# Kernel tuning notes

Measured on AMD Instinct MI355X. Metric: run time of the kernel, lower is better.

Reference implementation:

```python
import jax, jax.numpy as jnp
import numpy as np

L, B, T, C, H, FF = 2, 2, 2048, 512, 8, 1024
HS = C // H  # head size
EPS = 1.1920929e-07  # torch float32 finfo eps (nn.RMSNorm default)


def setup_inputs() -> dict:
    key = jax.random.key(0)
    ks = jax.random.split(key, 20)
    s = 0.02
    return {
        "hidden": jax.random.normal(ks[0], (B, T, C), jnp.float32),
        "target": jax.random.normal(ks[1], (B, T, C), jnp.float32),
        # self-attn per-head projections (bias=False)
        "Wq_s": jax.random.normal(ks[2], (L, H, C, HS)) * s,
        "Wk_s": jax.random.normal(ks[3], (L, H, C, HS)) * s,
        "Wv_s": jax.random.normal(ks[4], (L, H, C, HS)) * s,
        "Wo_s": jax.random.normal(ks[5], (L, C, C)) * s,
        "bo_s": jnp.zeros((L, C)),
        # cross-attn per-head projections
        "Wq_x": jax.random.normal(ks[6], (L, H, C, HS)) * s,
        "Wk_x": jax.random.normal(ks[7], (L, H, C, HS)) * s,
        "Wv_x": jax.random.normal(ks[8], (L, H, C, HS)) * s,
        "Wo_x": jax.random.normal(ks[9], (L, C, C)) * s,
        "bo_x": jnp.zeros((L, C)),
        # FFN
        "W1": jax.random.normal(ks[10], (L, C, FF)) * s,
        "b1": jnp.zeros((L, FF)),
        "W2": jax.random.normal(ks[11], (L, FF, C)) * s,
        "b2": jnp.zeros((L, C)),
        # RMSNorm gains ln1..ln4
        "g1": jnp.ones((L, C)),
        "g2": jnp.ones((L, C)),
        "g3": jnp.ones((L, C)),
        "g4": jnp.ones((L, C)),
    }


def _rms(x, g):
    return x * jax.lax.rsqrt(jnp.mean(x * x, axis=-1, keepdims=True) + EPS) * g


def _attn(q_in, kv_in, Wq, Wk, Wv, Wo, bo, causal):
    # q_in: [B,Tq,C], kv_in: [B,Tk,C]; W*: [H,C,HS]
    q = jnp.einsum('btc,hcd->bhtd', q_in, Wq)
    k = jnp.einsum('bsc,hcd->bhsd', kv_in, Wk)
    v = jnp.einsum('bsc,hcd->bhsd', kv_in, Wv)
    wei = jnp.einsum('bhtd,bhsd->bhts', q, k) * (HS ** -0.5)  # [B,H,Tq,Tk]
    if causal:
        Tq, Tk = q_in.shape[1], kv_in.shape[1]
        mask = jnp.tril(jnp.ones((Tq, Tk), bool))
        wei = jnp.where(mask, wei, -jnp.inf)
    wei = jax.nn.softmax(wei, axis=-1)
    out = jnp.einsum('bhts,bhsd->bhtd', wei, v)
    out = out.transpose(0, 2, 1, 3).reshape(q_in.shape[0], q_in.shape[1], C)
    return out @ Wo + bo


def reference(hidden, target, Wq_s, Wk_s, Wv_s, Wo_s, bo_s,
              Wq_x, Wk_x, Wv_x, Wo_x, bo_x,
              W1, b1, W2, b2, g1, g2, g3, g4):
    t = target
    for l in range(L):
        # masked self-attention with RMSNorm pre-norm + residual
        t = t + _attn(_rms(t, g1[l]), _rms(t, g1[l]), Wq_s[l], Wk_s[l], Wv_s[l],
                      Wo_s[l], bo_s[l], causal=True)
        # cross-attention: K/V from ln2(hidden), Q from ln3(t)
        t = t + _attn(_rms(t, g3[l]), _rms(hidden, g2[l]), Wq_x[l], Wk_x[l], Wv_x[l],
                      Wo_x[l], bo_x[l], causal=False)
        # GELU FFN
        h = _rms(t, g4[l])
        t = t + (jax.nn.gelu(h @ W1[l] + b1[l], approximate=False) @ W2[l] + b2[l])
    return t
```

## Files before the change

kernel.cpp:

```cpp
#include <hip/hip_runtime.h>
#include <hip/hip_bf16.h>
#include <math.h>

#define L 2
#define B 2
#define T 2048
#define C 512
#define H 8
#define FF 1024
#define HS 64
#define EPSV 1.1920929e-07f

typedef __hip_bfloat16 bf16;
typedef __attribute__((ext_vector_type(8))) short short8;
typedef __attribute__((ext_vector_type(4))) float f32x4;

__device__ __forceinline__ float b2f(bf16 x) { return __bfloat162float(x); }

__device__ __forceinline__ void gl16(const unsigned short* g, unsigned short* l) {
    __builtin_amdgcn_global_load_lds(
        (const __attribute__((address_space(1))) unsigned int*)g,
        (__attribute__((address_space(3))) unsigned int*)l, 16, 0, 0);
}

__global__ void detect_k(const unsigned short* __restrict__ g1bits, int* __restrict__ flag) {
    if (threadIdx.x == 0 && blockIdx.x == 0)
        *flag = (g1bits[0] != (unsigned short)0x3F80u) ? 1 : 0;
}

__device__ __forceinline__ float ld_in(const void* p, size_t i, int fl) {
    return fl ? ((const float*)p)[i] : b2f(((const bf16*)p)[i]);
}

#define QKVT_TOT 1572864
#define WO_TOT 524288
#define W12_TOT 1048576
#define SM_TOT 9216
#define ACT_TOT 2097152
#define PREP_TOT (2 * QKVT_TOT + 2 * WO_TOT + 2 * W12_TOT + SM_TOT + 2 * ACT_TOT)

struct PrepArgs {
    const void *Wq_s, *Wk_s, *Wv_s, *Wo_s, *Wq_x, *Wk_x, *Wv_x, *Wo_x, *W1, *W2;
    const void* sm[8];
    const void *hidden, *target;
    bf16 *cQKVs, *cQKVx, *cWoTs, *cWoTx, *cW1T, *cW2T, *smallDst;
    float *hid, *t_buf;
    const int* flag;
};

__global__ void prep_k(PrepArgs pa) {
    long long i = (long long)blockIdx.x * 256 + threadIdx.x;
    if (i >= PREP_TOT) return;
    int fl = *pa.flag;
    if (i < 2LL * QKVT_TOT) {
        int which = i >= QKVT_TOT;
        int j = (int)(i - (long long)which * QKVT_TOT);
        int l = j / 786432, r = j - l * 786432;
        int n = r >> 9, c = r & 511;
        int p = n >> 9, nn = n & 511;
        int hh = nn >> 6, d = nn & 63;
        const void* src = which ? (p == 0 ? pa.Wq_x : p == 1 ? pa.Wk_x : pa.Wv_x)
                                : (p == 0 ? pa.Wq_s : p == 1 ? pa.Wk_s : pa.Wv_s);
        size_t si = ((size_t)(l * 8 + hh) * 512 + c) * 64 + d;
        (which ? pa.cQKVx : pa.cQKVs)[j] = __float2bfloat16(ld_in(src, si, fl));
        return;
    }
    i -= 2LL * QKVT_TOT;
    if (i < 2LL * WO_TOT) {
        int which = i >= WO_TOT;
        int j = (int)(i - (long long)which * WO_TOT);
        int l = j >> 18, r = j & 262143;
        int n = r >> 9, c = r & 511;
        size_t si = ((size_t)l << 18) + ((size_t)c << 9) + n;
        (which ? pa.cWoTx : pa.cWoTs)[j] = __float2bfloat16(ld_in(which ? pa.Wo_x : pa.Wo_s, si, fl));
        return;
    }
    i -= 2LL * WO_TOT;
    if (i < W12_TOT) {
        int j = (int)i;
        int l = j >> 19, r = j & 524287;
        int n = r >> 9, c = r & 511;
        size_t si = ((size_t)l << 19) + ((size_t)c << 10) + n;
        pa.cW1T[j] = __float2bfloat16(ld_in(pa.W1, si, fl));
        return;
    }
    i -= W12_TOT;
    if (i < W12_TOT) {
        int j = (int)i;
        int l = j >> 19, r = j & 524287;
        int n = r >> 10, c = r & 1023;
        size_t si = ((size_t)l << 19) + ((size_t)c << 9) + n;
        pa.cW2T[j] = __float2bfloat16(ld_in(pa.W2, si, fl));
        return;
    }
    i -= W12_TOT;
    if (i < SM_TOT) {
        int j = (int)i;
        const int cum[9] = {0, 1024, 2048, 4096, 5120, 6144, 7168, 8192, 9216};
        int k = 0;
        while (j >= cum[k + 1]) k++;
        pa.smallDst[j] = __float2bfloat16(ld_in(pa.sm[k], j - cum[k], fl));
        return;
    }
    i -= SM_TOT;
    if (i < ACT_TOT) {
        pa.hid[i] = ld_in(pa.hidden, (size_t)i, fl);
    } else {
        size_t j = i - ACT_TOT;
        pa.t_buf[j] = ld_in(pa.target, j, fl);
    }
}

__global__ void write_out_k(const float* __restrict__ in, void* __restrict__ out, int n,
                            const int* __restrict__ flag) {
    int i = blockIdx.x * blockDim.x + threadIdx.x;
    if (i >= n) return;
    if (*flag) ((float*)out)[i] = in[i];
    else       ((bf16*)out)[i] = __float2bfloat16(in[i]);
}

__global__ void rmsnorm_k(const float* __restrict__ x, const bf16* __restrict__ g,
                          bf16* __restrict__ y) {
    int row = blockIdx.x;
    int tid = threadIdx.x;
    const float* xr = x + (size_t)row * C;
    float v0 = xr[tid], v1 = xr[tid + 256];
    __shared__ float red[256];
    red[tid] = v0 * v0 + v1 * v1;
    __syncthreads();
    for (int s = 128; s > 0; s >>= 1) {
        if (tid < s) red[tid] += red[tid + s];
        __syncthreads();
    }
    float sc = rsqrtf(red[0] / (float)C + EPSV);
    y[(size_t)row * C + tid] = __float2bfloat16(v0 * sc * b2f(g[tid]));
    y[(size_t)row * C + tid + 256] = __float2bfloat16(v1 * sc * b2f(g[tid + 256]));
}

__global__ void rmsnorm2_k(const float* __restrict__ xa, const bf16* __restrict__ ga,
                           bf16* __restrict__ ya, const float* __restrict__ xb,
                           const bf16* __restrict__ gb, bf16* __restrict__ yb) {
    int sel = blockIdx.y;
    const float* x = sel ? xb : xa;
    const bf16* g = sel ? gb : ga;
    bf16* y = sel ? yb : ya;
    int row = blockIdx.x;
    int tid = threadIdx.x;
    const float* xr = x + (size_t)row * C;
    float v0 = xr[tid], v1 = xr[tid + 256];
    __shared__ float red[256];
    red[tid] = v0 * v0 + v1 * v1;
    __syncthreads();
    for (int s = 128; s > 0; s >>= 1) {
        if (tid < s) red[tid] += red[tid + s];
        __syncthreads();
    }
    float sc = rsqrtf(red[0] / (float)C + EPSV);
    y[(size_t)row * C + tid] = __float2bfloat16(v0 * sc * b2f(g[tid]));
    y[(size_t)row * C + tid + 256] = __float2bfloat16(v1 * sc * b2f(g[tid + 256]));
}

#define GPAD 40
struct GDesc {
    const bf16* A; const bf16* Bt; const bf16* bias; float* resid; bf16* out;
    int N, K, ldOut, ep, nblkx, blkofs;
};
struct GBatch { GDesc d[3]; int nd; };

__global__ __launch_bounds__(256) void gemm_batch_k(GBatch gb) {
    int bid = blockIdx.x;
    int di = 0;
    if (gb.nd > 1 && bid >= gb.d[1].blkofs) di = 1;
    if (gb.nd > 2 && bid >= gb.d[2].blkofs) di = 2;
    GDesc g = gb.d[di];
    int lb = bid - g.blkofs;
    int bx = lb % g.nblkx, by = lb / g.nblkx;
    int m0 = by * 64, n0 = bx * 64;

    __shared__ unsigned short As[2][64 * GPAD], Bs[2][64 * GPAD];
    int tid = threadIdx.x, lane = tid & 63, wave = tid >> 6;
    int wr = wave >> 1, wc = wave & 1, quad = lane >> 4, l15 = lane & 15;
    const unsigned short* Au = (const unsigned short*)g.A;
    const unsigned short* Bu = (const unsigned short*)g.Bt;

    int srow = tid >> 2;
    int sseg = tid & 3;
    const unsigned short* agp = Au + (size_t)(m0 + srow) * g.K + sseg * 8;
    const unsigned short* bgp = Bu + (size_t)(n0 + srow) * g.K + sseg * 8;
    int soff = srow * GPAD + sseg * 8;

    short8 va = *(const short8*)agp;
    short8 vb = *(const short8*)bgp;
    *(short8*)(&As[0][soff]) = va;
    *(short8*)(&Bs[0][soff]) = vb;

    f32x4 zf = {0.f, 0.f, 0.f, 0.f};
    f32x4 acc[2][2];
    acc[0][0] = zf; acc[0][1] = zf; acc[1][0] = zf; acc[1][1] = zf;

    int ra0 = wr * 32 + l15, ra1 = ra0 + 16;
    int rb0 = wc * 32 + l15, rb1 = rb0 + 16;
    int oa0 = ra0 * GPAD + quad * 8;
    int oa1 = ra1 * GPAD + quad * 8;
    int ob0 = rb0 * GPAD + quad * 8;
    int ob1 = rb1 * GPAD + quad * 8;

    int nk = g.K >> 5;
    __syncthreads();
    for (int kt = 0; kt < nk; kt++) {
        int cur = kt & 1;
        if (kt + 1 < nk) {
            va = *(const short8*)(agp + (kt + 1) * 32);
            vb = *(const short8*)(bgp + (kt + 1) * 32);
        }
        short8 a0 = *(const short8*)(&As[cur][oa0]);
        short8 a1 = *(const short8*)(&As[cur][oa1]);
        short8 b0 = *(const short8*)(&Bs[cur][ob0]);
        short8 b1 = *(const short8*)(&Bs[cur][ob1]);
        acc[0][0] = __builtin_amdgcn_mfma_f32_16x16x32_bf16(a0, b0, acc[0][0], 0, 0, 0);
        acc[0][1] = __builtin_amdgcn_mfma_f32_16x16x32_bf16(a0, b1, acc[0][1], 0, 0, 0);
        acc[1][0] = __builtin_amdgcn_mfma_f32_16x16x32_bf16(a1, b0, acc[1][0], 0, 0, 0);
        acc[1][1] = __builtin_amdgcn_mfma_f32_16x16x32_bf16(a1, b1, acc[1][1], 0, 0, 0);
        if (kt + 1 < nk) {
            *(short8*)(&As[cur ^ 1][soff]) = va;
            *(short8*)(&Bs[cur ^ 1][soff]) = vb;
        }
        __syncthreads();
    }

#pragma unroll
    for (int mi = 0; mi < 2; mi++) {
#pragma unroll
        for (int ni = 0; ni < 2; ni++) {
            int colg = n0 + wc * 32 + ni * 16 + l15;
            float bv = (g.ep == 1 || g.ep == 2) ? b2f(g.bias[colg]) : 0.f;
#pragma unroll
            for (int r2 = 0; r2 < 4; r2++) {
                int rowg = m0 + wr * 32 + mi * 16 + quad * 4 + r2;
                float v = acc[mi][ni][r2];
                if (g.ep == 0) {
                    g.out[(size_t)rowg * g.ldOut + colg] = __float2bfloat16(v);
                } else if (g.ep == 1) {
                    g.resid[(size_t)rowg * g.ldOut + colg] += v + bv;
                } else if (g.ep == 2) {
                    float u = v + bv;
                    g.out[(size_t)rowg * g.ldOut + colg] =
                        __float2bfloat16(0.5f * u * (1.f + erff(u * 0.70710678118654752f)));
                } else {
                    g.out[((size_t)((colg >> 11) * 512 + rowg) << 11) + (colg & 2047)] =
                        __float2bfloat16(v);
                }
            }
        }
    }
}

#define PST 72
__global__ __launch_bounds__(256) void attn_mfma_k(const bf16* __restrict__ qkv,
                                                   const bf16* __restrict__ vT,
                                                   bf16* __restrict__ attnout, int causal) {
    __shared__ unsigned short KsA[2][4096], VtA[2][4096];
    __shared__ unsigned short Ps[4][16 * PST];
    int qt = causal ? (gridDim.x - 1 - blockIdx.x) : blockIdx.x;
    int h = blockIdx.y, b = blockIdx.z;
    int tid = threadIdx.x, lane = tid & 63, w = tid >> 6;
    int quad = lane >> 4, l15 = lane & 15;
    const unsigned short* qk = (const unsigned short*)qkv;
    const unsigned short* vTp = (const unsigned short*)vT + ((size_t)b * 512 + h * 64) * T;
    size_t rowbase = (size_t)b * T;
    int koff = 512 + h * 64;
    unsigned short* Pw = Ps[w];
    bf16* Pwb = (bf16*)Pw;

    const unsigned short* qrow = qk + (rowbase + qt * 64 + w * 16 + l15) * 1536 + h * 64;
    short8 aq0 = *(const short8*)(qrow + quad * 8);
    short8 aq1 = *(const short8*)(qrow + 32 + quad * 8);

    int srow = lane >> 3;
    int ssp = (lane & 7) ^ (srow & 7);

    f32x4 zf = {0.f, 0.f, 0.f, 0.f};
    f32x4 oacc[4];
#pragma unroll
    for (int i = 0; i < 4; i++) oacc[i] = zf;
    float lpart[4] = {0.f, 0.f, 0.f, 0.f};

    int nT = causal ? (qt + 1) : (T / 64);

#pragma unroll
    for (int j = 0; j < 2; j++) {
        int c = w * 2 + j;
        int r = c * 8 + srow;
        gl16(qk + (rowbase + r) * 1536 + koff + ssp * 8, KsA[0] + c * 512);
        gl16(vTp + (size_t)r * T + ssp * 8, VtA[0] + c * 512);
    }
    __syncthreads();

    int buf = 0;
    for (int st = 0; st < nT; st++) {
        if (st + 1 < nT) {
#pragma unroll
            for (int j = 0; j < 2; j++) {
                int c = w * 2 + j;
                int r = c * 8 + srow;
                gl16(qk + (rowbase + (st + 1) * 64 + r) * 1536 + koff + ssp * 8,
                     KsA[buf ^ 1] + c * 512);
                gl16(vTp + (size_t)r * T + (st + 1) * 64 + ssp * 8, VtA[buf ^ 1] + c * 512);
            }
        }

        const unsigned short* Kb = KsA[buf];
        const unsigned short* Vb = VtA[buf];

        f32x4 sacc[4];
#pragma unroll
        for (int i = 0; i < 4; i++) sacc[i] = zf;
#pragma unroll
        for (int ni = 0; ni < 4; ni++) {
            int rr = ni * 16 + l15;
            short8 bk0 = *(const short8*)(Kb + rr * 64 + ((quad ^ (rr & 7)) * 8));
            short8 bk1 = *(const short8*)(Kb + rr * 64 + (((4 + quad) ^ (rr & 7)) * 8));
            sacc[ni] = __builtin_amdgcn_mfma_f32_16x16x32_bf16(aq0, bk0, sacc[ni], 0, 0, 0);
            sacc[ni] = __builtin_amdgcn_mfma_f32_16x16x32_bf16(aq1, bk1, sacc[ni], 0, 0, 0);
        }

        bool diag = causal && (st == qt);
        int qrl = w * 16 + quad * 4;
#pragma unroll
        for (int reg = 0; reg < 4; reg++) {
            float lp = 0.f;
#pragma unroll
            for (int ni = 0; ni < 4; ni++) {
                int s_l = ni * 16 + l15;
                float p = __expf(sacc[ni][reg] * 0.125f);
                if (diag && s_l > qrl + reg) p = 0.f;
                lp += p;
                Pwb[(quad * 4 + reg) * PST + s_l] = __float2bfloat16(p);
            }
            lpart[reg] += lp;
        }

        short8 ap0 = *(const short8*)(Pw + l15 * PST + quad * 8);
        short8 ap1 = *(const short8*)(Pw + l15 * PST + 32 + quad * 8);
#pragma unroll
        for (int dj = 0; dj < 4; dj++) {
            int rr = dj * 16 + l15;
            short8 bv0 = *(const short8*)(Vb + rr * 64 + ((quad ^ (rr & 7)) * 8));
            short8 bv1 = *(const short8*)(Vb + rr * 64 + (((4 + quad) ^ (rr & 7)) * 8));
            oacc[dj] = __builtin_amdgcn_mfma_f32_16x16x32_bf16(ap0, bv0, oacc[dj], 0, 0, 0);
            oacc[dj] = __builtin_amdgcn_mfma_f32_16x16x32_bf16(ap1, bv1, oacc[dj], 0, 0, 0);
        }

        __syncthreads();
        buf ^= 1;
    }

#pragma unroll
    for (int reg = 0; reg < 4; reg++) {
#pragma unroll
        for (int mk = 1; mk < 16; mk <<= 1) lpart[reg] += __shfl_xor(lpart[reg], mk, 64);
        lpart[reg] = 1.0f / lpart[reg];
    }
#pragma unroll
    for (int dj = 0; dj < 4; dj++) {
        int d = dj * 16 + l15;
#pragma unroll
        for (int reg = 0; reg < 4; reg++) {
            int q = w * 16 + quad * 4 + reg;
            attnout[(rowbase + qt * 64 + q) * C + h * HS + d] =
                __float2bfloat16(oacc[dj][reg] * lpart[reg]);
        }
    }
}

extern "C" void kernel_launch(void* const* d_in, const int* in_sizes, int n_in,
                              void* d_out, int out_size, void* d_ws, size_t ws_size,
                              hipStream_t stream) {
    const int BTC = B * T * C;
    const int BTF = B * T * FF;

    char* wsb = (char*)d_ws;
    int* flag = (int*)wsb;
    bf16* cur = (bf16*)(wsb + 256);
    bf16* cQKVs = cur;   cur += QKVT_TOT;
    bf16* cQKVx = cur;   cur += QKVT_TOT;
    bf16* cWoTs = cur;   cur += WO_TOT;
    bf16* cWoTx = cur;   cur += WO_TOT;
    bf16* cW1T = cur;    cur += W12_TOT;
    bf16* cW2T = cur;    cur += W12_TOT;
    bf16* smallBase = cur;
    bf16* cbo_s = cur;   cur += L * C;
    bf16* cbo_x = cur;   cur += L * C;
    bf16* cb1 = cur;     cur += L * FF;
    bf16* cb2 = cur;     cur += L * C;
    bf16* cg1 = cur;     cur += L * C;
    bf16* cg2 = cur;     cur += L * C;
    bf16* cg3 = cur;     cur += L * C;
    bf16* cg4 = cur;     cur += L * C;
    bf16* n1 = cur;      cur += BTC;
    bf16* n2 = cur;      cur += BTC;
    bf16* qkvbuf = cur;  cur += B * T * 3 * C;
    bf16* vTbuf = cur;   cur += BTC;
    bf16* attnout = cur; cur += BTC;
    bf16* h1buf = cur;   cur += BTF;
    size_t f32_off = (((char*)cur - wsb) + 255) & ~(size_t)255;
    float* t_buf = (float*)(wsb + f32_off);
    float* hid = t_buf + BTC;

    dim3 blk256(256);
    detect_k<<<1, 64, 0, stream>>>((const unsigned short*)d_in[16], flag);

    PrepArgs pa;
    pa.Wq_s = d_in[2]; pa.Wk_s = d_in[3]; pa.Wv_s = d_in[4]; pa.Wo_s = d_in[5];
    pa.Wq_x = d_in[7]; pa.Wk_x = d_in[8]; pa.Wv_x = d_in[9]; pa.Wo_x = d_in[10];
    pa.W1 = d_in[12]; pa.W2 = d_in[14];
    pa.sm[0] = d_in[6];  pa.sm[1] = d_in[11]; pa.sm[2] = d_in[13]; pa.sm[3] = d_in[15];
    pa.sm[4] = d_in[16]; pa.sm[5] = d_in[17]; pa.sm[6] = d_in[18]; pa.sm[7] = d_in[19];
    pa.hidden = d_in[0]; pa.target = d_in[1];
    pa.cQKVs = cQKVs; pa.cQKVx = cQKVx; pa.cWoTs = cWoTs; pa.cWoTx = cWoTx;
    pa.cW1T = cW1T; pa.cW2T = cW2T; pa.smallDst = smallBase;
    pa.hid = hid; pa.t_buf = t_buf; pa.flag = flag;
    prep_k<<<(PREP_TOT + 255) / 256, blk256, 0, stream>>>(pa);

    const int M = B * T;
    dim3 attngrid(T / 64, H, B);

    for (int l = 0; l < L; l++) {
        bf16* qkvW_s = cQKVs + (size_t)l * 3 * C * C;
        bf16* qkvW_x = cQKVx + (size_t)l * 3 * C * C;
        bf16* woT_s = cWoTs + (size_t)l * C * C;
        bf16* woT_x = cWoTx + (size_t)l * C * C;
        bf16* w1T = cW1T + (size_t)l * C * FF;
        bf16* w2T = cW2T + (size_t)l * FF * C;

        rmsnorm_k<<<M, blk256, 0, stream>>>(t_buf, cg1 + l * C, n1);
        {
            GBatch gb;
            gb.nd = 2;
            gb.d[0] = {n1, qkvW_s, nullptr, nullptr, qkvbuf, 1024, C, 3 * C, 0, 16, 0};
            gb.d[1] = {qkvW_s + (size_t)1024 * C, n1, nullptr, nullptr, vTbuf,
                       M, C, 0, 3, 64, 1024};
            gemm_batch_k<<<1024 + 512, blk256, 0, stream>>>(gb);
        }
        attn_mfma_k<<<attngrid, blk256, 0, stream>>>(qkvbuf, vTbuf, attnout, 1);
        {
            GBatch gb;
            gb.nd = 1;
            gb.d[0] = {attnout, woT_s, cbo_s + l * C, t_buf, nullptr, C, C, C, 1, 8, 0};
            gemm_batch_k<<<512, blk256, 0, stream>>>(gb);
        }

        rmsnorm2_k<<<dim3(M, 2), blk256, 0, stream>>>(t_buf, cg3 + l * C, n1, hid, cg2 + l * C, n2);
        {
            GBatch gb;
            gb.nd = 3;
            gb.d[0] = {n1, qkvW_x, nullptr, nullptr, qkvbuf, C, C, 3 * C, 0, 8, 0};
            gb.d[1] = {n2, qkvW_x + (size_t)512 * C, nullptr, nullptr, qkvbuf + C,
                       C, C, 3 * C, 0, 8, 512};
            gb.d[2] = {qkvW_x + (size_t)1024 * C, n2, nullptr, nullptr, vTbuf,
                       M, C, 0, 3, 64, 1024};
            gemm_batch_k<<<512 + 512 + 512, blk256, 0, stream>>>(gb);
        }
        attn_mfma_k<<<attngrid, blk256, 0, stream>>>(qkvbuf, vTbuf, attnout, 0);
        {
            GBatch gb;
            gb.nd = 1;
            gb.d[0] = {attnout, woT_x, cbo_x + l * C, t_buf, nullptr, C, C, C, 1, 8, 0};
            gemm_batch_k<<<512, blk256, 0, stream>>>(gb);
        }

        rmsnorm_k<<<M, blk256, 0, stream>>>(t_buf, cg4 + l * C, n1);
        {
            GBatch gb;
            gb.nd = 1;
            gb.d[0] = {n1, w1T, cb1 + l * FF, nullptr, h1buf, FF, C, FF, 2, 16, 0};
            gemm_batch_k<<<1024, blk256, 0, stream>>>(gb);
        }
        {
            GBatch gb;
            gb.nd = 1;
            gb.d[0] = {h1buf, w2T, cb2 + l * C, t_buf, nullptr, C, FF, C, 1, 8, 0};
            gemm_batch_k<<<512, blk256, 0, stream>>>(gb);
        }
    }

    write_out_k<<<(BTC + 255) / 256, blk256, 0, stream>>>(t_buf, d_out, BTC, flag);
}
```

Before: 548.6 us.

## Split attention KV loop across two blocks and combine partials in a separate kernel

Each attention block now handles only every other KV tile (interleaved by a new grid z index), which doubles the number of blocks. It writes unnormalized fp32 partial outputs and row sums, and a new combine kernel adds them and normalizes. The softmax scale times log2(e) is folded into Q in the QKV GEMM epilogue so the kernel can use exp2f, and the causal mask is moved into a separate diagonal-only branch. The double-buffered async prefetch is replaced by a single buffer with two barriers per tile, giving up load/compute overlap. It also adds fp32 partial traffic and an extra kernel launch per attention.

```diff
diff --git a/kernel.cpp b/kernel.cpp
--- a/kernel.cpp
+++ b/kernel.cpp
@@ -10,6 +10,7 @@
 #define FF 1024
 #define HS 64
 #define EPSV 1.1920929e-07f
+#define QSCALE 0.18033688011112042f
 
 typedef __hip_bfloat16 bf16;
 typedef __attribute__((ext_vector_type(8))) short short8;
@@ -246,6 +247,8 @@
                     float u = v + bv;
                     g.out[(size_t)rowg * g.ldOut + colg] =
                         __float2bfloat16(0.5f * u * (1.f + erff(u * 0.70710678118654752f)));
+                } else if (g.ep == 4) {
+                    g.out[(size_t)rowg * g.ldOut + colg] = __float2bfloat16(v * QSCALE);
                 } else {
                     g.out[((size_t)((colg >> 11) * 512 + rowg) << 11) + (colg & 2047)] =
                         __float2bfloat16(v);
@@ -258,11 +261,13 @@
 #define PST 72
 __global__ __launch_bounds__(256) void attn_mfma_k(const bf16* __restrict__ qkv,
                                                    const bf16* __restrict__ vT,
-                                                   bf16* __restrict__ attnout, int causal) {
-    __shared__ unsigned short KsA[2][4096], VtA[2][4096];
+                                                   float* __restrict__ Opart,
+                                                   float* __restrict__ Lpart, int causal) {
+    __shared__ unsigned short Ks[4096], Vt[4096];
     __shared__ unsigned short Ps[4][16 * PST];
     int qt = causal ? (gridDim.x - 1 - blockIdx.x) : blockIdx.x;
-    int h = blockIdx.y, b = blockIdx.z;
+    int h = blockIdx.y, bz = blockIdx.z;
+    int b = bz >> 1, jc = bz & 1;
     int tid = threadIdx.x, lane = tid & 63, w = tid >> 6;
     int quad = lane >> 4, l15 = lane & 15;
     const unsigned short* qk = (const unsigned short*)qkv;
@@ -286,31 +291,16 @@
     float lpart[4] = {0.f, 0.f, 0.f, 0.f};
 
     int nT = causal ? (qt + 1) : (T / 64);
-
-#pragma unroll
-    for (int j = 0; j < 2; j++) {
-        int c = w * 2 + j;
-        int r = c * 8 + srow;
-        gl16(qk + (rowbase + r) * 1536 + koff + ssp * 8, KsA[0] + c * 512);
-        gl16(vTp + (size_t)r * T + ssp * 8, VtA[0] + c * 512);
-    }
-    __syncthreads();
-
-    int buf = 0;
-    for (int st = 0; st < nT; st++) {
-        if (st + 1 < nT) {
-#pragma unroll
-            for (int j = 0; j < 2; j++) {
-                int c = w * 2 + j;
-                int r = c * 8 + srow;
-                gl16(qk + (rowbase + (st + 1) * 64 + r) * 1536 + koff + ssp * 8,
-                     KsA[buf ^ 1] + c * 512);
-                gl16(vTp + (size_t)r * T + (st + 1) * 64 + ssp * 8, VtA[buf ^ 1] + c * 512);
-            }
-        }
-
-        const unsigned short* Kb = KsA[buf];
-        const unsigned short* Vb = VtA[buf];
+    for (int st = jc; st < nT; st += 2) {
+        __syncthreads();
+#pragma unroll
+        for (int j2 = 0; j2 < 2; j2++) {
+            int c = w * 2 + j2;
+            int r = c * 8 + srow;
+            gl16(qk + (rowbase + st * 64 + r) * 1536 + koff + ssp * 8, Ks + c * 512);
+            gl16(vTp + (size_t)r * T + st * 64 + ssp * 8, Vt + c * 512);
+        }
+        __syncthreads();
 
         f32x4 sacc[4];
 #pragma unroll
@@ -318,26 +308,40 @@
 #pragma unroll
         for (int ni = 0; ni < 4; ni++) {
             int rr = ni * 16 + l15;
-            short8 bk0 = *(const short8*)(Kb + rr * 64 + ((quad ^ (rr & 7)) * 8));
-            short8 bk1 = *(const short8*)(Kb + rr * 64 + (((4 + quad) ^ (rr & 7)) * 8));
+            short8 bk0 = *(const short8*)(Ks + rr * 64 + ((quad ^ (rr & 7)) * 8));
+            short8 bk1 = *(const short8*)(Ks + rr * 64 + (((4 + quad) ^ (rr & 7)) * 8));
             sacc[ni] = __builtin_amdgcn_mfma_f32_16x16x32_bf16(aq0, bk0, sacc[ni], 0, 0, 0);
             sacc[ni] = __builtin_amdgcn_mfma_f32_16x16x32_bf16(aq1, bk1, sacc[ni], 0, 0, 0);
         }
 
-        bool diag = causal && (st == qt);
-        int qrl = w * 16 + quad * 4;
-#pragma unroll
-        for (int reg = 0; reg < 4; reg++) {
-            float lp = 0.f;
-#pragma unroll
-            for (int ni = 0; ni < 4; ni++) {
-                int s_l = ni * 16 + l15;
-                float p = __expf(sacc[ni][reg] * 0.125f);
-                if (diag && s_l > qrl + reg) p = 0.f;
-                lp += p;
-                Pwb[(quad * 4 + reg) * PST + s_l] = __float2bfloat16(p);
+        if (causal && st == qt) {
+            int qrl = w * 16 + quad * 4;
+#pragma unroll
+            for (int reg = 0; reg < 4; reg++) {
+                float lp = 0.f;
+#pragma unroll
+                for (int ni = 0; ni < 4; ni++) {
+                    int s_l = ni * 16 + l15;
+                    float p = exp2f(sacc[ni][reg]);
+                    if (s_l > qrl + reg) p = 0.f;
+                    lp += p;
+                    Pwb[(quad * 4 + reg) * PST + s_l] = __float2bfloat16(p);
+                }
+                lpart[reg] += lp;
             }
-            lpart[reg] += lp;
+        } else {
+#pragma unroll
+            for (int reg = 0; reg < 4; reg++) {
+                float lp = 0.f;
+#pragma unroll
+                for (int ni = 0; ni < 4; ni++) {
+                    int s_l = ni * 16 + l15;
+                    float p = exp2f(sacc[ni][reg]);
+                    lp += p;
+                    Pwb[(quad * 4 + reg) * PST + s_l] = __float2bfloat16(p);
+                }
+                lpart[reg] += lp;
+            }
         }
 
         short8 ap0 = *(const short8*)(Pw + l15 * PST + quad * 8);
@@ -345,32 +349,46 @@
 #pragma unroll
         for (int dj = 0; dj < 4; dj++) {
             int rr = dj * 16 + l15;
-            short8 bv0 = *(const short8*)(Vb + rr * 64 + ((quad ^ (rr & 7)) * 8));
-            short8 bv1 = *(const short8*)(Vb + rr * 64 + (((4 + quad) ^ (rr & 7)) * 8));
+            short8 bv0 = *(const short8*)(Vt + rr * 64 + ((quad ^ (rr & 7)) * 8));
+            short8 bv1 = *(const short8*)(Vt + rr * 64 + (((4 + quad) ^ (rr & 7)) * 8));
             oacc[dj] = __builtin_amdgcn_mfma_f32_16x16x32_bf16(ap0, bv0, oacc[dj], 0, 0, 0);
             oacc[dj] = __builtin_amdgcn_mfma_f32_16x16x32_bf16(ap1, bv1, oacc[dj], 0, 0, 0);
         }
-
-        __syncthreads();
-        buf ^= 1;
     }
 
 #pragma unroll
     for (int reg = 0; reg < 4; reg++) {
 #pragma unroll
         for (int mk = 1; mk < 16; mk <<= 1) lpart[reg] += __shfl_xor(lpart[reg], mk, 64);
-        lpart[reg] = 1.0f / lpart[reg];
-    }
+    }
+    if (l15 == 0) {
+        int lbase = jc * (B * H * T) + ((b * H + h) * T) + qt * 64 + w * 16 + quad * 4;
+#pragma unroll
+        for (int reg = 0; reg < 4; reg++) Lpart[lbase + reg] = lpart[reg];
+    }
+    float* Ob = Opart + (size_t)jc * (B * T * C);
 #pragma unroll
     for (int dj = 0; dj < 4; dj++) {
         int d = dj * 16 + l15;
 #pragma unroll
         for (int reg = 0; reg < 4; reg++) {
             int q = w * 16 + quad * 4 + reg;
-            attnout[(rowbase + qt * 64 + q) * C + h * HS + d] =
-                __float2bfloat16(oacc[dj][reg] * lpart[reg]);
-        }
-    }
+            Ob[(rowbase + qt * 64 + q) * C + h * HS + d] = oacc[dj][reg];
+        }
+    }
+}
+
+__global__ void attn_comb_k(const float* __restrict__ Opart, const float* __restrict__ Lpart,
+                            bf16* __restrict__ attnout) {
+    int idx = blockIdx.x * 256 + threadIdx.x;
+    int c = idx & 511;
+    int h = c >> 6;
+    int bt = idx >> 9;
+    int b = bt >> 11, t = bt & 2047;
+    int li = (b * H + h) * T + t;
+    float l0 = Lpart[li], l1 = Lpart[B * H * T + li];
+    float inv = 1.0f / (l0 + l1);
+    attnout[idx] = __float2bfloat16((Opart[idx] + Opart[(size_t)B * T * C + idx]) * inv);
 }
 
 extern "C" void kernel_launch(void* const* d_in, const int* in_sizes, int n_in,
@@ -406,6 +424,8 @@
     size_t f32_off = (((char*)cur - wsb) + 255) & ~(size_t)255;
     float* t_buf = (float*)(wsb + f32_off);
     float* hid = t_buf + BTC;
+    float* Opart = hid + BTC;
+    float* Lpart = Opart + 2 * BTC;
 
     dim3 blk256(256);
     detect_k<<<1, 64, 0, stream>>>((const unsigned short*)d_in[16], flag);
@@ -423,7 +443,7 @@
     prep_k<<<(PREP_TOT + 255) / 256, blk256, 0, stream>>>(pa);
 
     const int M = B * T;
-    dim3 attngrid(T / 64, H, B);
+    dim3 attngrid(T / 64, H, B * 2);
 
     for (int l = 0; l < L; l++) {
         bf16* qkvW_s = cQKVs + (size_t)l * 3 * C * C;
@@ -436,13 +456,16 @@
         rmsnorm_k<<<M, blk256, 0, stream>>>(t_buf, cg1 + l * C, n1);
         {
             GBatch gb;
-            gb.nd = 2;
-            gb.d[0] = {n1, qkvW_s, nullptr, nullptr, qkvbuf, 1024, C, 3 * C, 0, 16, 0};
-            gb.d[1] = {qkvW_s + (size_t)1024 * C, n1, nullptr, nullptr, vTbuf,
+            gb.nd = 3;
+            gb.d[0] = {n1, qkvW_s, nullptr, nullptr, qkvbuf, C, C, 3 * C, 4, 8, 0};
+            gb.d[1] = {n1, qkvW_s + (size_t)512 * C, nullptr, nullptr, qkvbuf + C,
+                       C, C, 3 * C, 0, 8, 512};
+            gb.d[2] = {qkvW_s + (size_t)1024 * C, n1, nullptr, nullptr, vTbuf,
                        M, C, 0, 3, 64, 1024};
-            gemm_batch_k<<<1024 + 512, blk256, 0, stream>>>(gb);
-        }
-        attn_mfma_k<<<attngrid, blk256, 0, stream>>>(qkvbuf, vTbuf, attnout, 1);
+            gemm_batch_k<<<512 + 512 + 512, blk256, 0, stream>>>(gb);
+        }
+        attn_mfma_k<<<attngrid, blk256, 0, stream>>>(qkvbuf, vTbuf, Opart, Lpart, 1);
+        attn_comb_k<<<BTC / 256, blk256, 0, stream>>>(Opart, Lpart, attnout);
         {
             GBatch gb;
             gb.nd = 1;
@@ -454,14 +477,15 @@
         {
             GBatch gb;
             gb.nd = 3;
-            gb.d[0] = {n1, qkvW_x, nullptr, nullptr, qkvbuf, C, C, 3 * C, 0, 8, 0};
+            gb.d[0] = {n1, qkvW_x, nullptr, nullptr, qkvbuf, C, C, 3 * C, 4, 8, 0};
             gb.d[1] = {n2, qkvW_x + (size_t)512 * C, nullptr, nullptr, qkvbuf + C,
                        C, C, 3 * C, 0, 8, 512};
             gb.d[2] = {qkvW_x + (size_t)1024 * C, n2, nullptr, nullptr, vTbuf,
                        M, C, 0, 3, 64, 1024};
             gemm_batch_k<<<512 + 512 + 512, blk256, 0, stream>>>(gb);
         }
-        attn_mfma_k<<<attngrid, blk256, 0, stream>>>(qkvbuf, vTbuf, attnout, 0);
+        attn_mfma_k<<<attngrid, blk256, 0, stream>>>(qkvbuf, vTbuf, Opart, Lpart, 0);
+        attn_comb_k<<<BTC / 256, blk256, 0, stream>>>(Opart, Lpart, attnout);
         {
             GBatch gb;
             gb.nd = 1;
```

Result: slower. 566.4 us (+3.2%).

## Keep attention probabilities in registers via transposed S MFMA and prescale Q

Applied to the files above, without the earlier changes.

Computes the score tile transposed (K as A operand) so each lane's softmax probabilities line up with the B operand of a 16x16x16 MFMA for P·V. This drops the per-wave LDS staging buffer and the extra LDS round trip. Q is prescaled by log2(e)/sqrt(HS) in a new GEMM epilogue, so exp2f replaces __expf plus the multiply. The row-sum reduction shrinks to two shuffles, and the output is written with packed 4-wide stores. The cost is twice as many smaller MFMAs for P·V and an extra descriptor in the QKV GEMM batch.

```diff
diff --git a/kernel.cpp b/kernel.cpp
--- a/kernel.cpp
+++ b/kernel.cpp
@@ -10,12 +10,18 @@
 #define FF 1024
 #define HS 64
 #define EPSV 1.1920929e-07f
+#define QSCALE 0.18033688011112042f
 
 typedef __hip_bfloat16 bf16;
 typedef __attribute__((ext_vector_type(8))) short short8;
+typedef __attribute__((ext_vector_type(4))) short short4v;
 typedef __attribute__((ext_vector_type(4))) float f32x4;
 
 __device__ __forceinline__ float b2f(bf16 x) { return __bfloat162float(x); }
+__device__ __forceinline__ short f2bf_s(float f) {
+    bf16 t = __float2bfloat16(f);
+    return *reinterpret_cast<short*>(&t);
+}
 
 __device__ __forceinline__ void gl16(const unsigned short* g, unsigned short* l) {
     __builtin_amdgcn_global_load_lds(
@@ -246,6 +252,8 @@
                     float u = v + bv;
                     g.out[(size_t)rowg * g.ldOut + colg] =
                         __float2bfloat16(0.5f * u * (1.f + erff(u * 0.70710678118654752f)));
+                } else if (g.ep == 4) {
+                    g.out[(size_t)rowg * g.ldOut + colg] = __float2bfloat16(v * QSCALE);
                 } else {
                     g.out[((size_t)((colg >> 11) * 512 + rowg) << 11) + (colg & 2047)] =
                         __float2bfloat16(v);
@@ -255,12 +263,10 @@
     }
 }
 
-#define PST 72
 __global__ __launch_bounds__(256) void attn_mfma_k(const bf16* __restrict__ qkv,
                                                    const bf16* __restrict__ vT,
                                                    bf16* __restrict__ attnout, int causal) {
     __shared__ unsigned short KsA[2][4096], VtA[2][4096];
-    __shared__ unsigned short Ps[4][16 * PST];
     int qt = causal ? (gridDim.x - 1 - blockIdx.x) : blockIdx.x;
     int h = blockIdx.y, b = blockIdx.z;
     int tid = threadIdx.x, lane = tid & 63, w = tid >> 6;
@@ -269,8 +275,6 @@
     const unsigned short* vTp = (const unsigned short*)vT + ((size_t)b * 512 + h * 64) * T;
     size_t rowbase = (size_t)b * T;
     int koff = 512 + h * 64;
-    unsigned short* Pw = Ps[w];
-    bf16* Pwb = (bf16*)Pw;
 
     const unsigned short* qrow = qk + (rowbase + qt * 64 + w * 16 + l15) * 1536 + h * 64;
     short8 aq0 = *(const short8*)(qrow + quad * 8);
@@ -283,13 +287,13 @@
     f32x4 oacc[4];
 #pragma unroll
     for (int i = 0; i < 4; i++) oacc[i] = zf;
-    float lpart[4] = {0.f, 0.f, 0.f, 0.f};
+    float lsum = 0.f;
 
     int nT = causal ? (qt + 1) : (T / 64);
 
 #pragma unroll
-    for (int j = 0; j < 2; j++) {
-        int c = w * 2 + j;
+    for (int j2 = 0; j2 < 2; j2++) {
+        int c = w * 2 + j2;
         int r = c * 8 + srow;
         gl16(qk + (rowbase + r) * 1536 + koff + ssp * 8, KsA[0] + c * 512);
         gl16(vTp + (size_t)r * T + ssp * 8, VtA[0] + c * 512);
@@ -297,18 +301,18 @@
     __syncthreads();
 
     int buf = 0;
+    int x7 = l15 & 7;
     for (int st = 0; st < nT; st++) {
         if (st + 1 < nT) {
 #pragma unroll
-            for (int j = 0; j < 2; j++) {
-                int c = w * 2 + j;
+            for (int j2 = 0; j2 < 2; j2++) {
+                int c = w * 2 + j2;
                 int r = c * 8 + srow;
                 gl16(qk + (rowbase + (st + 1) * 64 + r) * 1536 + koff + ssp * 8,
                      KsA[buf ^ 1] + c * 512);
                 gl16(vTp + (size_t)r * T + (st + 1) * 64 + ssp * 8, VtA[buf ^ 1] + c * 512);
             }
         }
-
         const unsigned short* Kb = KsA[buf];
         const unsigned short* Vb = VtA[buf];
 
@@ -320,56 +324,62 @@
             int rr = ni * 16 + l15;
             short8 bk0 = *(const short8*)(Kb + rr * 64 + ((quad ^ (rr & 7)) * 8));
             short8 bk1 = *(const short8*)(Kb + rr * 64 + (((4 + quad) ^ (rr & 7)) * 8));
-            sacc[ni] = __builtin_amdgcn_mfma_f32_16x16x32_bf16(aq0, bk0, sacc[ni], 0, 0, 0);
-            sacc[ni] = __builtin_amdgcn_mfma_f32_16x16x32_bf16(aq1, bk1, sacc[ni], 0, 0, 0);
-        }
-
-        bool diag = causal && (st == qt);
-        int qrl = w * 16 + quad * 4;
-#pragma unroll
-        for (int reg = 0; reg < 4; reg++) {
-            float lp = 0.f;
+            sacc[ni] = __builtin_amdgcn_mfma_f32_16x16x32_bf16(bk0, aq0, sacc[ni], 0, 0, 0);
+            sacc[ni] = __builtin_amdgcn_mfma_f32_16x16x32_bf16(bk1, aq1, sacc[ni], 0, 0, 0);
+        }
+
+        short4v pb[4];
+        if (causal && st == qt) {
+            int q_l = w * 16 + l15;
 #pragma unroll
             for (int ni = 0; ni < 4; ni++) {
-                int s_l = ni * 16 + l15;
-                float p = __expf(sacc[ni][reg] * 0.125f);
-                if (diag && s_l > qrl + reg) p = 0.f;
-                lp += p;
-                Pwb[(quad * 4 + reg) * PST + s_l] = __float2bfloat16(p);
+#pragma unroll
+                for (int reg = 0; reg < 4; reg++) {
+                    int s_l = ni * 16 + quad * 4 + reg;
+                    float p = (s_l > q_l) ? 0.f : exp2f(sacc[ni][reg]);
+                    lsum += p;
+                    pb[ni][reg] = f2bf_s(p);
+                }
             }
-            lpart[reg] += lp;
-        }
-
-        short8 ap0 = *(const short8*)(Pw + l15 * PST + quad * 8);
-        short8 ap1 = *(const short8*)(Pw + l15 * PST + 32 + quad * 8);
+        } else {
+#pragma unroll
+            for (int ni = 0; ni < 4; ni++) {
+#pragma unroll
+                for (int reg = 0; reg < 4; reg++) {
+                    float p = exp2f(sacc[ni][reg]);
+                    lsum += p;
+                    pb[ni][reg] = f2bf_s(p);
+                }
+            }
+        }
+
 #pragma unroll
         for (int dj = 0; dj < 4; dj++) {
-            int rr = dj * 16 + l15;
-            short8 bv0 = *(const short8*)(Vb + rr * 64 + ((quad ^ (rr & 7)) * 8));
-            short8 bv1 = *(const short8*)(Vb + rr * 64 + (((4 + quad) ^ (rr & 7)) * 8));
-            oacc[dj] = __builtin_amdgcn_mfma_f32_16x16x32_bf16(ap0, bv0, oacc[dj], 0, 0, 0);
-            oacc[dj] = __builtin_amdgcn_mfma_f32_16x16x32_bf16(ap1, bv1, oacc[dj], 0, 0, 0);
+            int rbase = (dj * 16 + l15) * 64;
+#pragma unroll
+            for (int ni = 0; ni < 4; ni++) {
+                int gp = (ni * 2 + (quad >> 1)) ^ x7;
+                short4v av = *(const short4v*)(Vb + rbase + gp * 8 + (quad & 1) * 4);
+                oacc[dj] =
+                    __builtin_amdgcn_mfma_f32_16x16x16bf16_1k(av, pb[ni], oacc[dj], 0, 0, 0);
+            }
         }
 
         __syncthreads();
         buf ^= 1;
     }
 
-#pragma unroll
-    for (int reg = 0; reg < 4; reg++) {
-#pragma unroll
-        for (int mk = 1; mk < 16; mk <<= 1) lpart[reg] += __shfl_xor(lpart[reg], mk, 64);
-        lpart[reg] = 1.0f / lpart[reg];
-    }
+    lsum += __shfl_xor(lsum, 16, 64);
+    lsum += __shfl_xor(lsum, 32, 64);
+    float inv = 1.0f / lsum;
+
+    bf16* orow = attnout + (rowbase + qt * 64 + w * 16 + l15) * C + h * HS;
 #pragma unroll
     for (int dj = 0; dj < 4; dj++) {
-        int d = dj * 16 + l15;
-#pragma unroll
-        for (int reg = 0; reg < 4; reg++) {
-            int q = w * 16 + quad * 4 + reg;
-            attnout[(rowbase + qt * 64 + q) * C + h * HS + d] =
-                __float2bfloat16(oacc[dj][reg] * lpart[reg]);
-        }
+        short4v ov;
+#pragma unroll
+        for (int reg = 0; reg < 4; reg++) ov[reg] = f2bf_s(oacc[dj][reg] * inv);
+        *(short4v*)(orow + dj * 16 + quad * 4) = ov;
     }
 }
 
@@ -436,11 +446,13 @@
         rmsnorm_k<<<M, blk256, 0, stream>>>(t_buf, cg1 + l * C, n1);
         {
             GBatch gb;
-            gb.nd = 2;
-            gb.d[0] = {n1, qkvW_s, nullptr, nullptr, qkvbuf, 1024, C, 3 * C, 0, 16, 0};
-            gb.d[1] = {qkvW_s + (size_t)1024 * C, n1, nullptr, nullptr, vTbuf,
+            gb.nd = 3;
+            gb.d[0] = {n1, qkvW_s, nullptr, nullptr, qkvbuf, C, C, 3 * C, 4, 8, 0};
+            gb.d[1] = {n1, qkvW_s + (size_t)512 * C, nullptr, nullptr, qkvbuf + C,
+                       C, C, 3 * C, 0, 8, 512};
+            gb.d[2] = {qkvW_s + (size_t)1024 * C, n1, nullptr, nullptr, vTbuf,
                        M, C, 0, 3, 64, 1024};
-            gemm_batch_k<<<1024 + 512, blk256, 0, stream>>>(gb);
+            gemm_batch_k<<<512 + 512 + 512, blk256, 0, stream>>>(gb);
         }
         attn_mfma_k<<<attngrid, blk256, 0, stream>>>(qkvbuf, vTbuf, attnout, 1);
         {
@@ -454,7 +466,7 @@
         {
             GBatch gb;
             gb.nd = 3;
-            gb.d[0] = {n1, qkvW_x, nullptr, nullptr, qkvbuf, C, C, 3 * C, 0, 8, 0};
+            gb.d[0] = {n1, qkvW_x, nullptr, nullptr, qkvbuf, C, C, 3 * C, 4, 8, 0};
             gb.d[1] = {n2, qkvW_x + (size_t)512 * C, nullptr, nullptr, qkvbuf + C,
                        C, C, 3 * C, 0, 8, 512};
             gb.d[2] = {qkvW_x + (size_t)1024 * C, n2, nullptr, nullptr, vTbuf,
```

Result: slower. 579.3 us (+5.6%).
